# Kernel tuning notes

Hardware: AMD Instinct MI355X
Metric: run time of the kernel (lower is better)

## Reference

```python
import jax, jax.numpy as jnp
import numpy as np

EPS = 1e-5

def setup_inputs() -> dict:
    key = jax.random.key(0)
    ks = jax.random.split(key, 12)
    B = 4096
    x = jax.random.normal(ks[0], (B, 28, 28, 1), dtype=jnp.float32)
    # BatchNorm1d(1) affine params (applied per-channel over active sites)
    bn_gamma = jnp.ones((1,), jnp.float32)
    bn_beta = jnp.zeros((1,), jnp.float32)
    # SubMConv2d weights, HWIO layout
    w1 = jax.random.normal(ks[1], (3, 3, 1, 32), jnp.float32) * 0.1
    b1 = jax.random.normal(ks[2], (32,), jnp.float32) * 0.01
    w2 = jax.random.normal(ks[3], (3, 3, 32, 64), jnp.float32) * 0.05
    b2 = jax.random.normal(ks[4], (64,), jnp.float32) * 0.01
    # FC layers (torch Linear: y = x @ W.T + b)
    fcw1 = jax.random.normal(ks[5], (128, 14 * 14 * 64), jnp.float32) * 0.01
    fcb1 = jnp.zeros((128,), jnp.float32)
    fcw2 = jax.random.normal(ks[6], (10, 128), jnp.float32) * 0.05
    fcb2 = jnp.zeros((10,), jnp.float32)
    return {"x": x, "bn_gamma": bn_gamma, "bn_beta": bn_beta,
            "w1": w1, "b1": b1, "w2": w2, "b2": b2,
            "fcw1": fcw1, "fcb1": fcb1, "fcw2": fcw2, "fcb2": fcb2}

def _subm_conv(feat, mask, w, b):
    # Submanifold conv: inactive inputs are zero (already masked), and the
    # output coordinate set equals the input active set -> mask the output.
    y = jax.lax.conv_general_dilated(
        feat, w, window_strides=(1, 1), padding='SAME',
        dimension_numbers=('NHWC', 'HWIO', 'NHWC'))
    return jnp.where(mask, y + b, 0.0)

def reference(x, bn_gamma, bn_beta, w1, b1, w2, b2, fcw1, fcb1, fcw2, fcb2):
    # from_dense: active sites are locations with nonzero feature. [B,28,28,1]
    mask = (x != 0)  # single channel -> site mask [B,28,28,1]
    maskf = mask.astype(x.dtype)
    # BatchNorm1d(1) on the [N_active, 1] sparse feature tensor (batch stats)
    n = jnp.maximum(maskf.sum(), 1.0)
    mean = (x * maskf).sum() / n
    var = (jnp.square(x - mean) * maskf).sum() / n
    feat = maskf * (bn_gamma * (x - mean) * jax.lax.rsqrt(var + EPS) + bn_beta)
    # SubMConv2d(1,32,3,1) + ReLU
    h = jax.nn.relu(_subm_conv(feat, mask, w1, b1))  # [B,28,28,32]
    # SubMConv2d(32,64,3,1) + ReLU
    h = jax.nn.relu(_subm_conv(h, mask, w2, b2))     # [B,28,28,64]
    # SparseMaxPool2d(2,2): max over active sites per window; since values are
    # post-ReLU (>=0) and inactive sites hold 0, dense maxpool is exact, and
    # fully-inactive windows correctly yield 0 after ToDense.
    h = jax.lax.reduce_window(h, -jnp.inf, jax.lax.max,
                              (1, 2, 2, 1), (1, 2, 2, 1), 'VALID')  # [B,14,14,64]
    # ToDense gives NCHW [B,64,14,14]; torch.flatten uses C-major order
    h = jnp.transpose(h, (0, 3, 1, 2)).reshape(h.shape[0], -1)  # [B,12544]
    # dropout1/dropout2 are identity in eval mode
    h = jax.nn.relu(h @ fcw1.T + fcb1)
    logits = h @ fcw2.T + fcb2
    return jax.nn.log_softmax(logits, axis=1)
```

## Files before the change

### kernel.cpp

```cpp
#include <hip/hip_runtime.h>
#include <stdint.h>

typedef unsigned short u16;
typedef unsigned int u32;
typedef __attribute__((ext_vector_type(8))) short bf16x8;
typedef __attribute__((ext_vector_type(4))) float f32x4;

__device__ __forceinline__ u16 f2bf(float f) {
    u32 u = __float_as_uint(f);
    u32 r = (u + 0x7fffu + ((u >> 16) & 1u)) >> 16;
    return (u16)r;
}

__device__ __forceinline__ void gload16(const u16* src, u16* dst) {
    __builtin_amdgcn_global_load_lds(
        (const __attribute__((address_space(1))) u32*)src,
        (__attribute__((address_space(3))) u32*)dst, 16, 0, 0);
}

__global__ __launch_bounds__(256) void k_stats(const float* __restrict__ x, int n,
                                               float* __restrict__ stats) {
    int t = blockIdx.x * 256 + threadIdx.x;
    int stride = gridDim.x * 256;
    float c = 0.f, s = 0.f, ss = 0.f;
    for (int i = t; i < n; i += stride) {
        float v = x[i];
        if (v != 0.f) { c += 1.f; s += v; ss = fmaf(v, v, ss); }
    }
    for (int off = 32; off > 0; off >>= 1) {
        c  += __shfl_down(c, off);
        s  += __shfl_down(s, off);
        ss += __shfl_down(ss, off);
    }
    __shared__ float red[3][4];
    int lane = threadIdx.x & 63, wv = threadIdx.x >> 6;
    if (lane == 0) { red[0][wv] = c; red[1][wv] = s; red[2][wv] = ss; }
    __syncthreads();
    if (threadIdx.x == 0) {
        atomicAdd(&stats[0], red[0][0] + red[0][1] + red[0][2] + red[0][3]);
        atomicAdd(&stats[1], red[1][0] + red[1][1] + red[1][2] + red[1][3]);
        atomicAdd(&stats[2], red[2][0] + red[2][1] + red[2][2] + red[2][3]);
    }
}

__global__ void k_finalize(const float* __restrict__ g, const float* __restrict__ b,
                           float* __restrict__ stats) {
    float n = stats[0]; if (n < 1.f) n = 1.f;
    float mean = stats[1] / n;
    float var = stats[2] / n - mean * mean;
    if (var < 0.f) var = 0.f;
    float scale = g[0] * rsqrtf(var + 1e-5f);
    stats[4] = scale;
    stats[5] = b[0] - mean * scale;
}

__global__ __launch_bounds__(256) void k_prepall(const float* __restrict__ w2,
    const float* __restrict__ fcw1, u16* __restrict__ w2b, u16* __restrict__ fcw1b, int n)
{
    int i = blockIdx.x * 256 + threadIdx.x;
    if (i < 9 * 64 * 32) {
        int tap = i >> 11, rem = i & 2047, co = rem >> 5, ci = rem & 31;
        w2b[i] = f2bf(w2[tap * 2048 + ci * 64 + co]);
    }
    if (i < n) fcw1b[i] = f2bf(fcw1[i]);
}

__global__ __launch_bounds__(256, 2) void k_conv(const float* __restrict__ x,
    const float* __restrict__ w1, const float* __restrict__ b1,
    const u16* __restrict__ w2b, const float* __restrict__ b2,
    const float* __restrict__ stats, u16* __restrict__ pooled)
{
    __shared__ u16 h1[28928];
    __shared__ float feat[30][30];
    __shared__ unsigned char mk[784];
    __shared__ unsigned char pm[200];
    const int t = threadIdx.x;
    const int b = blockIdx.x;
    const int lane = t & 63;
    const int wv = t >> 6;
    const int lg = lane >> 4;
    const int lr = lane & 15;

    const float scale = stats[4], shift = stats[5];

    for (int i = t; i < 14464; i += 256) ((u32*)h1)[i] = 0u;
    for (int i = t; i < 900; i += 256) (&feat[0][0])[i] = 0.f;
    __syncthreads();

    const float* xb = x + (size_t)b * 784;
    for (int i = t; i < 784; i += 256) {
        float v = xb[i];
        bool m = (v != 0.f);
        mk[i] = m ? 1 : 0;
        int h = i / 28, w = i - h * 28;
        feat[h + 1][w + 1] = m ? fmaf(v, scale, shift) : 0.f;
    }
    __syncthreads();

    if (t < 196) {
        int rr = t / 14, cc = t - rr * 14;
        int base = rr * 56 + cc * 2;
        pm[t] = (unsigned char)(mk[base] | (mk[base + 1] << 1)
              | (mk[base + 28] << 2) | (mk[base + 29] << 3));
    }

    {
        const int cp = (t >> 4) & 3;
        const int pxg = (t & 15) | ((t >> 6) << 4);
        float wk[9][8], bs[8];
        {
            float4 b0 = *(const float4*)(b1 + cp * 8);
            float4 b4 = *(const float4*)(b1 + cp * 8 + 4);
            bs[0]=b0.x; bs[1]=b0.y; bs[2]=b0.z; bs[3]=b0.w;
            bs[4]=b4.x; bs[5]=b4.y; bs[6]=b4.z; bs[7]=b4.w;
        }
        #pragma unroll
        for (int j = 0; j < 9; ++j) {
            float4 w0 = *(const float4*)(w1 + j * 32 + cp * 8);
            float4 w4 = *(const float4*)(w1 + j * 32 + cp * 8 + 4);
            wk[j][0]=w0.x; wk[j][1]=w0.y; wk[j][2]=w0.z; wk[j][3]=w0.w;
            wk[j][4]=w4.x; wk[j][5]=w4.y; wk[j][6]=w4.z; wk[j][7]=w4.w;
        }
        char* hb = (char*)h1 + cp * 14464;
        for (int px = pxg; px < 784; px += 64) {
            if (!mk[px]) continue;
            int h = px / 28, w = px - h * 28;
            float a[8];
            #pragma unroll
            for (int c = 0; c < 8; ++c) a[c] = bs[c];
            #pragma unroll
            for (int kh = 0; kh < 3; ++kh)
                #pragma unroll
                for (int kw = 0; kw < 3; ++kw) {
                    float f = feat[h + kh][w + kw];
                    #pragma unroll
                    for (int c = 0; c < 8; ++c) a[c] = fmaf(f, wk[kh * 3 + kw][c], a[c]);
                }
            u32 q0 = (u32)f2bf(fmaxf(a[0], 0.f)) | ((u32)f2bf(fmaxf(a[1], 0.f)) << 16);
            u32 q1 = (u32)f2bf(fmaxf(a[2], 0.f)) | ((u32)f2bf(fmaxf(a[3], 0.f)) << 16);
            u32 q2 = (u32)f2bf(fmaxf(a[4], 0.f)) | ((u32)f2bf(fmaxf(a[5], 0.f)) << 16);
            u32 q3 = (u32)f2bf(fmaxf(a[6], 0.f)) | ((u32)f2bf(fmaxf(a[7], 0.f)) << 16);
            *(uint4*)(hb + ((h + 1) * 30 + (w + 1)) * 16) = make_uint4(q0, q1, q2, q3);
        }
    }
    __syncthreads();

    bf16x8 wf[9][4];
    #pragma unroll
    for (int tap = 0; tap < 9; ++tap)
        #pragma unroll
        for (int nt = 0; nt < 4; ++nt)
            wf[tap][nt] = *(const bf16x8*)(w2b + tap * 2048 + (nt * 16 + lr) * 32 + lg * 8);
    float bias2[4];
    #pragma unroll
    for (int nt = 0; nt < 4; ++nt) bias2[nt] = b2[nt * 16 + lr];

    const int cb = wv & 1;
    const int r0 = wv >> 1;
    const char* gb = (const char*)h1 + lg * 14464 + (cb * 16 + lr) * 16;
    const bool store_ok = !(cb == 1 && lg == 3);
    const int pc0 = cb * 8 + lg * 2;
    u16* poolb = pooled + (size_t)b * 12544;

    #pragma unroll 1
    for (int i = 0; i < 7; ++i) {
        const int r = r0 + 2 * i;
        const char* ab = gb + 960 * r;
        bf16x8 a0[3], a1[3], a2[3], a3[3];
        #pragma unroll
        for (int kw = 0; kw < 3; ++kw) {
            a0[kw] = *(const bf16x8*)(ab + kw * 16);
            a1[kw] = *(const bf16x8*)(ab + 480 + kw * 16);
            a2[kw] = *(const bf16x8*)(ab + 960 + kw * 16);
        }
        f32x4 acc0[4], acc1[4];
        #pragma unroll
        for (int nt = 0; nt < 4; ++nt) {
            acc0[nt] = (f32x4){bias2[nt], bias2[nt], bias2[nt], bias2[nt]};
            acc1[nt] = acc0[nt];
        }
        #pragma unroll
        for (int nt = 0; nt < 4; ++nt)
            #pragma unroll
            for (int kw = 0; kw < 3; ++kw) {
                acc0[nt] = __builtin_amdgcn_mfma_f32_16x16x32_bf16(a0[kw], wf[kw][nt], acc0[nt], 0, 0, 0);
                acc0[nt] = __builtin_amdgcn_mfma_f32_16x16x32_bf16(a1[kw], wf[3 + kw][nt], acc0[nt], 0, 0, 0);
                acc0[nt] = __builtin_amdgcn_mfma_f32_16x16x32_bf16(a2[kw], wf[6 + kw][nt], acc0[nt], 0, 0, 0);
            }
        #pragma unroll
        for (int kw = 0; kw < 3; ++kw)
            a3[kw] = *(const bf16x8*)(ab + 1440 + kw * 16);
        #pragma unroll
        for (int nt = 0; nt < 4; ++nt)
            #pragma unroll
            for (int kw = 0; kw < 3; ++kw) {
                acc1[nt] = __builtin_amdgcn_mfma_f32_16x16x32_bf16(a1[kw], wf[kw][nt], acc1[nt], 0, 0, 0);
                acc1[nt] = __builtin_amdgcn_mfma_f32_16x16x32_bf16(a2[kw], wf[3 + kw][nt], acc1[nt], 0, 0, 0);
                acc1[nt] = __builtin_amdgcn_mfma_f32_16x16x32_bf16(a3[kw], wf[6 + kw][nt], acc1[nt], 0, 0, 0);
            }

        if (store_ok) {
            u32 pmw = *(const u16*)&pm[r * 14 + pc0];
            float m00 = (pmw & 1u)    ? 1.f : 0.f, m01 = (pmw & 2u)    ? 1.f : 0.f;
            float m10 = (pmw & 4u)    ? 1.f : 0.f, m11 = (pmw & 8u)    ? 1.f : 0.f;
            float n00 = (pmw & 256u)  ? 1.f : 0.f, n01 = (pmw & 512u)  ? 1.f : 0.f;
            float n10 = (pmw & 1024u) ? 1.f : 0.f, n11 = (pmw & 2048u) ? 1.f : 0.f;
            #pragma unroll
            for (int nt = 0; nt < 4; ++nt) {
                float p0 = fmaxf(fmaxf(fmaxf(acc0[nt][0], 0.f) * m00, fmaxf(acc0[nt][1], 0.f) * m01),
                                 fmaxf(fmaxf(acc1[nt][0], 0.f) * m10, fmaxf(acc1[nt][1], 0.f) * m11));
                float p1 = fmaxf(fmaxf(fmaxf(acc0[nt][2], 0.f) * n00, fmaxf(acc0[nt][3], 0.f) * n01),
                                 fmaxf(fmaxf(acc1[nt][2], 0.f) * n10, fmaxf(acc1[nt][3], 0.f) * n11));
                *(u32*)&poolb[(nt * 16 + lr) * 196 + r * 14 + pc0] =
                    (u32)f2bf(p0) | ((u32)f2bf(p1) << 16);
            }
        }
    }
}

__global__ __launch_bounds__(256, 4) void k_fc1(const u16* __restrict__ pooled,
    const u16* __restrict__ fcw1b, float* __restrict__ fc1, int M)
{
    __shared__ u16 Asm[8 * 64 * 8];
    __shared__ u16 Bsm[8 * 128 * 8];
    const int t = threadIdx.x;
    const int m0 = blockIdx.x * 64;
    const int kbase = blockIdx.y * 1792;
    const int lane = t & 63;
    const int wv = t >> 6;
    const int lg = lane >> 4, lr = lane & 15;
    const int wm = wv & 1, wn = wv >> 1;

    const int ia0 = t, ia1 = t + 256;
    const u16* as0 = pooled + (size_t)(m0 + (ia0 & 63)) * 12544 + (ia0 >> 6) * 8 + kbase;
    const u16* as1 = pooled + (size_t)(m0 + (ia1 & 63)) * 12544 + (ia1 >> 6) * 8 + kbase;
    const u16* bs0 = fcw1b + (size_t)(t & 127) * 12544 + ((t >> 7) + 0) * 8 + kbase;
    const u16* bs1 = fcw1b + (size_t)(t & 127) * 12544 + ((t >> 7) + 2) * 8 + kbase;
    const u16* bs2 = fcw1b + (size_t)(t & 127) * 12544 + ((t >> 7) + 4) * 8 + kbase;
    const u16* bs3 = fcw1b + (size_t)(t & 127) * 12544 + ((t >> 7) + 6) * 8 + kbase;
    u16* ad0 = &Asm[(size_t)ia0 * 8];
    u16* ad1 = &Asm[(size_t)ia1 * 8];
    u16* bd0 = &Bsm[(size_t)(t + 0) * 8];
    u16* bd1 = &Bsm[(size_t)(t + 256) * 8];
    u16* bd2 = &Bsm[(size_t)(t + 512) * 8];
    u16* bd3 = &Bsm[(size_t)(t + 768) * 8];

    f32x4 acc[2][4];
    #pragma unroll
    for (int mi = 0; mi < 2; ++mi)
        #pragma unroll
        for (int ni = 0; ni < 4; ++ni) acc[mi][ni] = (f32x4){0.f, 0.f, 0.f, 0.f};

    for (int s = 0; s < 28; ++s) {
        const int kk = s * 64;
        __syncthreads();
        gload16(as0 + kk, ad0);
        gload16(as1 + kk, ad1);
        gload16(bs0 + kk, bd0);
        gload16(bs1 + kk, bd1);
        gload16(bs2 + kk, bd2);
        gload16(bs3 + kk, bd3);
        asm volatile("s_waitcnt vmcnt(0)" ::: "memory");
        __syncthreads();
        #pragma unroll
        for (int ks = 0; ks < 2; ++ks) {
            bf16x8 a[2], bfr[4];
            #pragma unroll
            for (int mi = 0; mi < 2; ++mi)
                a[mi] = *(const bf16x8*)&Asm[(((ks * 4 + lg) * 64) + wm * 32 + mi * 16 + lr) * 8];
            #pragma unroll
            for (int ni = 0; ni < 4; ++ni)
                bfr[ni] = *(const bf16x8*)&Bsm[(((ks * 4 + lg) * 128) + wn * 64 + ni * 16 + lr) * 8];
            #pragma unroll
            for (int mi = 0; mi < 2; ++mi)
                #pragma unroll
                for (int ni = 0; ni < 4; ++ni)
                    acc[mi][ni] = __builtin_amdgcn_mfma_f32_16x16x32_bf16(a[mi], bfr[ni], acc[mi][ni], 0, 0, 0);
        }
    }

    #pragma unroll
    for (int mi = 0; mi < 2; ++mi)
        #pragma unroll
        for (int ni = 0; ni < 4; ++ni)
            #pragma unroll
            for (int q = 0; q < 4; ++q) {
                int m = m0 + wm * 32 + mi * 16 + lg * 4 + q;
                int n = wn * 64 + ni * 16 + lr;
                atomicAdd(&fc1[(size_t)m * 128 + n], acc[mi][ni][q]);
            }
}

__global__ __launch_bounds__(256) void k_fc2(const float* __restrict__ fc1,
    const float* __restrict__ fcb1, const float* __restrict__ fcw2,
    const float* __restrict__ fcb2, float* __restrict__ out, int M)
{
    __shared__ float red[8][32][10];
    const int t = threadIdx.x;
    const int ml = t & 31, kq = t >> 5;
    const int m = blockIdx.x * 32 + ml;
    float acc[10];
    #pragma unroll
    for (int c = 0; c < 10; ++c) acc[c] = 0.f;
    const float* fp = fc1 + (size_t)m * 128 + kq * 16;
    #pragma unroll
    for (int j = 0; j < 16; j += 4) {
        float4 v4 = *(const float4*)(fp + j);
        float vv[4] = {v4.x, v4.y, v4.z, v4.w};
        #pragma unroll
        for (int u = 0; u < 4; ++u) {
            int k = kq * 16 + j + u;
            float v = fmaxf(vv[u] + fcb1[k], 0.f);
            #pragma unroll
            for (int c = 0; c < 10; ++c) acc[c] = fmaf(v, fcw2[c * 128 + k], acc[c]);
        }
    }
    #pragma unroll
    for (int c = 0; c < 10; ++c) red[kq][ml][c] = acc[c];
    __syncthreads();
    if (kq == 0) {
        float lgt[10];
        #pragma unroll
        for (int c = 0; c < 10; ++c) {
            float sv = 0.f;
            #pragma unroll
            for (int s = 0; s < 8; ++s) sv += red[s][ml][c];
            lgt[c] = sv + fcb2[c];
        }
        float mx = lgt[0];
        #pragma unroll
        for (int c = 1; c < 10; ++c) mx = fmaxf(mx, lgt[c]);
        float se = 0.f;
        #pragma unroll
        for (int c = 0; c < 10; ++c) se += expf(lgt[c] - mx);
        float lse = mx + logf(se);
        #pragma unroll
        for (int c = 0; c < 10; ++c) out[(size_t)m * 10 + c] = lgt[c] - lse;
    }
}

extern "C" void kernel_launch(void* const* d_in, const int* in_sizes, int n_in,
                              void* d_out, int out_size, void* d_ws, size_t ws_size,
                              hipStream_t stream) {
    const float* x     = (const float*)d_in[0];
    const float* gamma = (const float*)d_in[1];
    const float* beta  = (const float*)d_in[2];
    const float* w1    = (const float*)d_in[3];
    const float* b1    = (const float*)d_in[4];
    const float* w2    = (const float*)d_in[5];
    const float* b2    = (const float*)d_in[6];
    const float* fcw1  = (const float*)d_in[7];
    const float* fcb1  = (const float*)d_in[8];
    const float* fcw2  = (const float*)d_in[9];
    const float* fcb2  = (const float*)d_in[10];
    float* out = (float*)d_out;

    const int B = in_sizes[0] / 784;

    float* stats  = (float*)d_ws;
    u16*   w2b    = (u16*)((char*)d_ws + 256);
    float* fc1    = (float*)((char*)d_ws + 256);
    u16*   pooled = (u16*)((char*)d_ws + 256 + (size_t)B * 128 * 4);
    u16*   fcw1b  = (u16*)((char*)d_ws + 256 + (size_t)B * 128 * 4 + (size_t)B * 12544 * 2);

    hipMemsetAsync(stats, 0, 32, stream);
    k_stats<<<1024, 256, 0, stream>>>(x, B * 784, stats);
    k_finalize<<<1, 1, 0, stream>>>(gamma, beta, stats);
    k_prepall<<<(128 * 12544 + 255) / 256, 256, 0, stream>>>(w2, fcw1, w2b, fcw1b, 128 * 12544);
    k_conv<<<B, 256, 0, stream>>>(x, w1, b1, w2b, b2, stats, pooled);
    hipMemsetAsync(fc1, 0, (size_t)B * 128 * 4, stream);
    k_fc1<<<dim3(B / 64, 7), 256, 0, stream>>>(pooled, fcw1b, fc1, B);
    k_fc2<<<B / 32, 256, 0, stream>>>(fc1, fcb1, fcw2, fcb2, out, B);
}
```

Before: 350.0 us.

## Split fused conv kernel into separate conv1 and conv2 kernels via global staging

Splits the fused conv kernel in two. The first computes conv1 with BN, ReLU and mask, writes padded bf16 activations and per-window pool masks to workspace, and runs at higher occupancy. The second streams those activations into LDS with async global-to-LDS loads and runs the MFMA conv2 with pooling. The goal is to drop the serial conv1 phase from the LDS-heavy MFMA kernel, at the cost of a roughly 237MB global round trip. It falls back to the fused kernel when the workspace is too small.

```diff
diff --git a/kernel.cpp b/kernel.cpp
--- a/kernel.cpp
+++ b/kernel.cpp
@@ -10,6 +10,12 @@
     u32 u = __float_as_uint(f);
     u32 r = (u + 0x7fffu + ((u >> 16) & 1u)) >> 16;
     return (u16)r;
+}
+
+__device__ __forceinline__ u32 cvtpk(float lo, float hi) {
+    u32 r;
+    asm("v_cvt_pk_bf16_f32 %0, %1, %2" : "=v"(r) : "v"(lo), "v"(hi));
+    return r;
 }
 
 __device__ __forceinline__ void gload16(const u16* src, u16* dst) {
@@ -63,6 +69,188 @@
         w2b[i] = f2bf(w2[tap * 2048 + ci * 64 + co]);
     }
     if (i < n) fcw1b[i] = f2bf(fcw1[i]);
+}
+
+__global__ __launch_bounds__(256, 4) void k_conv1(const float* __restrict__ x,
+    const float* __restrict__ w1, const float* __restrict__ b1,
+    const float* __restrict__ stats, u16* __restrict__ h1g,
+    unsigned char* __restrict__ pmg)
+{
+    __shared__ float feat[30][30];
+    __shared__ unsigned char mk[784];
+    const int t = threadIdx.x;
+    const int b = blockIdx.x;
+    const float scale = stats[4], shift = stats[5];
+
+    for (int i = t; i < 900; i += 256) (&feat[0][0])[i] = 0.f;
+    __syncthreads();
+    const float* xb = x + (size_t)b * 784;
+    for (int i = t; i < 784; i += 256) {
+        float v = xb[i];
+        bool m = (v != 0.f);
+        mk[i] = m ? 1 : 0;
+        int h = i / 28, w = i - h * 28;
+        feat[h + 1][w + 1] = m ? fmaf(v, scale, shift) : 0.f;
+    }
+    __syncthreads();
+
+    u16* hb_img = h1g + (size_t)b * 28928;
+
+    if (t < 196) {
+        int rr = t / 14, cc = t - rr * 14;
+        int base = rr * 56 + cc * 2;
+        pmg[(size_t)b * 200 + t] = (unsigned char)(mk[base] | (mk[base + 1] << 1)
+              | (mk[base + 28] << 2) | (mk[base + 29] << 3));
+    }
+    if (t < 120) {
+        int slot;
+        if (t < 30)       slot = t;
+        else if (t < 60)  slot = 840 + t;
+        else if (t < 88)  slot = (t - 59) * 30;
+        else if (t < 116) slot = (t - 87) * 30 + 29;
+        else              slot = 784 + t;
+        const uint4 z = make_uint4(0u, 0u, 0u, 0u);
+        #pragma unroll
+        for (int g = 0; g < 4; ++g)
+            *(uint4*)&hb_img[g * 7232 + slot * 8] = z;
+    }
+
+    const int cp = (t >> 4) & 3;
+    const int pxg = (t & 15) | ((t >> 6) << 4);
+    float wk[9][8], bs[8];
+    {
+        float4 b0 = *(const float4*)(b1 + cp * 8);
+        float4 b4 = *(const float4*)(b1 + cp * 8 + 4);
+        bs[0]=b0.x; bs[1]=b0.y; bs[2]=b0.z; bs[3]=b0.w;
+        bs[4]=b4.x; bs[5]=b4.y; bs[6]=b4.z; bs[7]=b4.w;
+    }
+    #pragma unroll
+    for (int j = 0; j < 9; ++j) {
+        float4 w0 = *(const float4*)(w1 + j * 32 + cp * 8);
+        float4 w4 = *(const float4*)(w1 + j * 32 + cp * 8 + 4);
+        wk[j][0]=w0.x; wk[j][1]=w0.y; wk[j][2]=w0.z; wk[j][3]=w0.w;
+        wk[j][4]=w4.x; wk[j][5]=w4.y; wk[j][6]=w4.z; wk[j][7]=w4.w;
+    }
+    u16* hb = hb_img + cp * 7232;
+    for (int px = pxg; px < 784; px += 64) {
+        int h = px / 28, w = px - h * 28;
+        float a[8];
+        #pragma unroll
+        for (int c = 0; c < 8; ++c) a[c] = bs[c];
+        #pragma unroll
+        for (int kh = 0; kh < 3; ++kh)
+            #pragma unroll
+            for (int kw = 0; kw < 3; ++kw) {
+                float f = feat[h + kh][w + kw];
+                #pragma unroll
+                for (int c = 0; c < 8; ++c) a[c] = fmaf(f, wk[kh * 3 + kw][c], a[c]);
+            }
+        float mf = mk[px] ? 1.f : 0.f;
+        u32 q0 = cvtpk(fmaxf(a[0], 0.f) * mf, fmaxf(a[1], 0.f) * mf);
+        u32 q1 = cvtpk(fmaxf(a[2], 0.f) * mf, fmaxf(a[3], 0.f) * mf);
+        u32 q2 = cvtpk(fmaxf(a[4], 0.f) * mf, fmaxf(a[5], 0.f) * mf);
+        u32 q3 = cvtpk(fmaxf(a[6], 0.f) * mf, fmaxf(a[7], 0.f) * mf);
+        *(uint4*)&hb[((h + 1) * 30 + (w + 1)) * 8] = make_uint4(q0, q1, q2, q3);
+    }
+}
+
+__global__ __launch_bounds__(256, 2) void k_conv2(const u16* __restrict__ h1g,
+    const unsigned char* __restrict__ pmg, const u16* __restrict__ w2b,
+    const float* __restrict__ b2, u16* __restrict__ pooled)
+{
+    __shared__ u16 h1[28928];
+    __shared__ unsigned char pm[200];
+    const int t = threadIdx.x;
+    const int b = blockIdx.x;
+    const int lane = t & 63;
+    const int wv = t >> 6;
+    const int lg = lane >> 4;
+    const int lr = lane & 15;
+
+    const u16* src = h1g + (size_t)b * 28928;
+    #pragma unroll
+    for (int i = 0; i < 14; ++i)
+        gload16(src + (i * 256 + t) * 8, &h1[(i * 256 + t) * 8]);
+    if (t < 32) {
+        uint4 v = *(const uint4*)(src + (3584 + t) * 8);
+        *(uint4*)&h1[(3584 + t) * 8] = v;
+    }
+    if (t < 50) ((u32*)pm)[t] = ((const u32*)(pmg + (size_t)b * 200))[t];
+
+    bf16x8 wf[9][4];
+    #pragma unroll
+    for (int tap = 0; tap < 9; ++tap)
+        #pragma unroll
+        for (int nt = 0; nt < 4; ++nt)
+            wf[tap][nt] = *(const bf16x8*)(w2b + tap * 2048 + (nt * 16 + lr) * 32 + lg * 8);
+    float bias2[4];
+    #pragma unroll
+    for (int nt = 0; nt < 4; ++nt) bias2[nt] = b2[nt * 16 + lr];
+
+    asm volatile("s_waitcnt vmcnt(0)" ::: "memory");
+    __syncthreads();
+
+    const int cb = wv & 1;
+    const int r0 = wv >> 1;
+    const char* gb = (const char*)h1 + lg * 14464 + (cb * 16 + lr) * 16;
+    const bool store_ok = !(cb == 1 && lg == 3);
+    const int pc0 = cb * 8 + lg * 2;
+    u16* poolb = pooled + (size_t)b * 12544;
+
+    #pragma unroll 1
+    for (int i = 0; i < 7; ++i) {
+        const int r = r0 + 2 * i;
+        const char* ab = gb + 960 * r;
+        bf16x8 a0[3], a1[3], a2[3], a3[3];
+        #pragma unroll
+        for (int kw = 0; kw < 3; ++kw) {
+            a0[kw] = *(const bf16x8*)(ab + kw * 16);
+            a1[kw] = *(const bf16x8*)(ab + 480 + kw * 16);
+            a2[kw] = *(const bf16x8*)(ab + 960 + kw * 16);
+        }
+        f32x4 acc0[4], acc1[4];
+        #pragma unroll
+        for (int nt = 0; nt < 4; ++nt) {
+            acc0[nt] = (f32x4){bias2[nt], bias2[nt], bias2[nt], bias2[nt]};
+            acc1[nt] = acc0[nt];
+        }
+        #pragma unroll
+        for (int nt = 0; nt < 4; ++nt)
+            #pragma unroll
+            for (int kw = 0; kw < 3; ++kw) {
+                acc0[nt] = __builtin_amdgcn_mfma_f32_16x16x32_bf16(a0[kw], wf[kw][nt], acc0[nt], 0, 0, 0);
+                acc0[nt] = __builtin_amdgcn_mfma_f32_16x16x32_bf16(a1[kw], wf[3 + kw][nt], acc0[nt], 0, 0, 0);
+                acc0[nt] = __builtin_amdgcn_mfma_f32_16x16x32_bf16(a2[kw], wf[6 + kw][nt], acc0[nt], 0, 0, 0);
+            }
+        #pragma unroll
+        for (int kw = 0; kw < 3; ++kw)
+            a3[kw] = *(const bf16x8*)(ab + 1440 + kw * 16);
+        #pragma unroll
+        for (int nt = 0; nt < 4; ++nt)
+            #pragma unroll
+            for (int kw = 0; kw < 3; ++kw) {
+                acc1[nt] = __builtin_amdgcn_mfma_f32_16x16x32_bf16(a1[kw], wf[kw][nt], acc1[nt], 0, 0, 0);
+                acc1[nt] = __builtin_amdgcn_mfma_f32_16x16x32_bf16(a2[kw], wf[3 + kw][nt], acc1[nt], 0, 0, 0);
+                acc1[nt] = __builtin_amdgcn_mfma_f32_16x16x32_bf16(a3[kw], wf[6 + kw][nt], acc1[nt], 0, 0, 0);
+            }
+
+        if (store_ok) {
+            u32 pmw = *(const u16*)&pm[r * 14 + pc0];
+            float m00 = (pmw & 1u)    ? 1.f : 0.f, m01 = (pmw & 2u)    ? 1.f : 0.f;
+            float m10 = (pmw & 4u)    ? 1.f : 0.f, m11 = (pmw & 8u)    ? 1.f : 0.f;
+            float n00 = (pmw & 256u)  ? 1.f : 0.f, n01 = (pmw & 512u)  ? 1.f : 0.f;
+            float n10 = (pmw & 1024u) ? 1.f : 0.f, n11 = (pmw & 2048u) ? 1.f : 0.f;
+            #pragma unroll
+            for (int nt = 0; nt < 4; ++nt) {
+                float p0 = fmaxf(fmaxf(fmaxf(acc0[nt][0], 0.f) * m00, fmaxf(acc0[nt][1], 0.f) * m01),
+                                 fmaxf(fmaxf(acc1[nt][0], 0.f) * m10, fmaxf(acc1[nt][1], 0.f) * m11));
+                float p1 = fmaxf(fmaxf(fmaxf(acc0[nt][2], 0.f) * n00, fmaxf(acc0[nt][3], 0.f) * n01),
+                                 fmaxf(fmaxf(acc1[nt][2], 0.f) * n10, fmaxf(acc1[nt][3], 0.f) * n11));
+                *(u32*)&poolb[(nt * 16 + lr) * 196 + r * 14 + pc0] =
+                    (u32)f2bf(p0) | ((u32)f2bf(p1) << 16);
+            }
+        }
+    }
 }
 
 __global__ __launch_bounds__(256, 2) void k_conv(const float* __restrict__ x,
@@ -357,17 +545,32 @@
 
     const int B = in_sizes[0] / 784;
 
-    float* stats  = (float*)d_ws;
-    u16*   w2b    = (u16*)((char*)d_ws + 256);
-    float* fc1    = (float*)((char*)d_ws + 256);
-    u16*   pooled = (u16*)((char*)d_ws + 256 + (size_t)B * 128 * 4);
-    u16*   fcw1b  = (u16*)((char*)d_ws + 256 + (size_t)B * 128 * 4 + (size_t)B * 12544 * 2);
+    char* base = (char*)d_ws;
+    float* stats  = (float*)base;
+    u16*   w2b    = (u16*)(base + 256);
+    float* fc1    = (float*)(base + 256);
+    size_t off_pooled = 256 + (size_t)B * 128 * 4;
+    u16*   pooled = (u16*)(base + off_pooled);
+    size_t off_fcw1b = off_pooled + (size_t)B * 12544 * 2;
+    u16*   fcw1b  = (u16*)(base + off_fcw1b);
+    size_t off_pmg = off_fcw1b + (size_t)128 * 12544 * 2;
+    unsigned char* pmg = (unsigned char*)(base + off_pmg);
+    size_t off_h1g = off_pmg + (size_t)B * 200;
+    u16*   h1g    = (u16*)(base + off_h1g);
+    size_t need_split = off_h1g + (size_t)B * 57856;
 
     hipMemsetAsync(stats, 0, 32, stream);
     k_stats<<<1024, 256, 0, stream>>>(x, B * 784, stats);
     k_finalize<<<1, 1, 0, stream>>>(gamma, beta, stats);
     k_prepall<<<(128 * 12544 + 255) / 256, 256, 0, stream>>>(w2, fcw1, w2b, fcw1b, 128 * 12544);
-    k_conv<<<B, 256, 0, stream>>>(x, w1, b1, w2b, b2, stats, pooled);
+
+    if (ws_size >= need_split) {
+        k_conv1<<<B, 256, 0, stream>>>(x, w1, b1, stats, h1g, pmg);
+        k_conv2<<<B, 256, 0, stream>>>(h1g, pmg, w2b, b2, pooled);
+    } else {
+        k_conv<<<B, 256, 0, stream>>>(x, w1, b1, w2b, b2, stats, pooled);
+    }
+
     hipMemsetAsync(fc1, 0, (size_t)B * 128 * 4, stream);
     k_fc1<<<dim3(B / 64, 7), 256, 0, stream>>>(pooled, fcw1b, fc1, B);
     k_fc2<<<B / 32, 256, 0, stream>>>(fc1, fcb1, fcw2, fcb2, out, B);
```

Measured after the change: 354.1 us. Within noise of the previous version (+1.2%).
